# Optimization experiments

Measured on AMD Instinct MI355X. Metric: run time of the kernel, lower is better.

## Reference

```python
import jax, jax.numpy as jnp
import numpy as np

TOP_K = 2
SCALING = 32.0 / 16.0  # lora_alpha / r

N, D, O = 4096, 4096, 4096   # tokens, in_features, out_features
E, H, R_RANK = 8, 3, 16      # experts, B-heads per expert, lora rank
W_SCALE = 0.02               # keep logits in a sane range


def setup_inputs() -> dict:
    key = jax.random.key(0)
    ks = jax.random.split(key, 6)
    return {
        "x": jax.random.normal(ks[0], (N, D), jnp.float32),
        "base_W": jax.random.normal(ks[1], (D, O), jnp.float32) * W_SCALE,
        "router_W": jax.random.normal(ks[2], (E, D), jnp.float32) * W_SCALE,
        "A": jax.random.normal(ks[3], (E, D, R_RANK), jnp.float32) * W_SCALE,
        "B": jax.random.normal(ks[4], (E, H, R_RANK, O), jnp.float32) * W_SCALE,
        "R": jax.random.normal(ks[5], (E, D, H), jnp.float32) * W_SCALE,
    }


def reference(x, base_W, router_W, A, B, R):
    # Base dense layer
    base = x @ base_W                                   # [N, O]
    # Expert router: softmax over experts, top-k gate renormalized
    probs = jax.nn.softmax(x @ router_W.T, axis=-1)     # [N, E]
    topv, topi = jax.lax.top_k(probs, TOP_K)            # [N, k]
    topv = topv / topv.sum(-1, keepdims=True)
    n_idx = jnp.arange(x.shape[0])[:, None]
    gate = jnp.zeros_like(probs).at[n_idx, topi].set(topv)  # dense [N, E] gate, 0 off top-k
    # Shared lora_A per expert
    a = jnp.einsum('nd,edr->ner', x, A)                 # [N, E, r]
    # Per-expert head router over lora_B heads
    head_w = jax.nn.softmax(jnp.einsum('nd,edh->neh', x, R), axis=-1)  # [N, E, H]
    # Head-weighted B projections, combined with expert gates
    delta = jnp.einsum('ner,neh,ehro,ne->no', a, head_w, B, gate)      # [N, O]
    return base + SCALING * delta
```

## Files before the change

kernel.cpp:

```cpp
#include <hip/hip_runtime.h>
#include <hip/hip_bf16.h>
#include <math.h>

typedef __bf16 bf16_t;
typedef __bf16 bf16x4_t __attribute__((ext_vector_type(4)));
typedef __bf16 bf16x8_t __attribute__((ext_vector_type(8)));
typedef float  f32x4_t  __attribute__((ext_vector_type(4)));

#define N_TOK 4096
#define D_IN  4096
#define O_OUT 4096
#define NEXP  8
#define NHEAD 3
#define RANK  16
#define KC2   384
#define PCOLS 256
#define NKZ   8
#define SCALING_F 2.0f


__device__ __forceinline__ void transpose_tile(const float* __restrict__ src,
                                               bf16_t* __restrict__ dst,
                                               int Rr, int Cc, int r0, int c0,
                                               float (*tile)[65]) {
  int q  = threadIdx.x & 15;
  int r4 = threadIdx.x >> 4;
  #pragma unroll
  for (int g = 0; g < 4; ++g) {
    int r = r4 + g * 16;
    float4 v = *(const float4*)(src + (size_t)(r0 + r) * Cc + c0 + q * 4);
    tile[r][q * 4 + 0] = v.x; tile[r][q * 4 + 1] = v.y;
    tile[r][q * 4 + 2] = v.z; tile[r][q * 4 + 3] = v.w;
  }
  __syncthreads();
  int j  = threadIdx.x & 7;
  int cc = threadIdx.x >> 3;
  #pragma unroll
  for (int h = 0; h < 2; ++h) {
    int c = cc + h * 32;
    bf16x8_t o;
    #pragma unroll
    for (int i = 0; i < 8; ++i) o[i] = (bf16_t)tile[j * 8 + i][c];
    *(bf16x8_t*)(dst + (size_t)(c0 + c) * Rr + r0 + j * 8) = o;
  }
}

__global__ __launch_bounds__(256) void prep_kernel(const float* __restrict__ x,
                                                   const float* __restrict__ base_W,
                                                   const float* __restrict__ rw,
                                                   const float* __restrict__ A,
                                                   const float* __restrict__ B,
                                                   const float* __restrict__ Rm,
                                                   bf16_t* __restrict__ xb,
                                                   bf16_t* __restrict__ WbT,
                                                   bf16_t* __restrict__ BbT,
                                                   bf16_t* __restrict__ PabT,
                                                   int* __restrict__ gidx,
                                                   float* __restrict__ gwv) {
  __shared__ float tile[64][65];
  int b = blockIdx.x;
  if (b < 4096) {
    transpose_tile(base_W, WbT, 4096, 4096, (b & 63) * 64, (b >> 6) * 64, tile);
  } else if (b < 5120) {
    int lane = threadIdx.x & 63;
    int wv = threadIdx.x >> 6;
    int n = (b - 4096) * 4 + wv;
    const float4* xv = (const float4*)(x + (size_t)n * D_IN);
    bf16x4_t* xo = (bf16x4_t*)(xb + (size_t)n * D_IN);
    float acc[NEXP] = {0, 0, 0, 0, 0, 0, 0, 0};
    for (int d = lane; d < D_IN / 4; d += 64) {
      float4 xx = xv[d];
      bf16x4_t ob = { (bf16_t)xx.x, (bf16_t)xx.y, (bf16_t)xx.z, (bf16_t)xx.w };
      xo[d] = ob;
      #pragma unroll
      for (int e = 0; e < NEXP; ++e) {
        float4 ww = ((const float4*)(rw + (size_t)e * D_IN))[d];
        acc[e] += xx.x * ww.x + xx.y * ww.y + xx.z * ww.z + xx.w * ww.w;
      }
    }
    #pragma unroll
    for (int e = 0; e < NEXP; ++e) {
      float v = acc[e];
      #pragma unroll
      for (int o = 32; o > 0; o >>= 1) v += __shfl_down(v, o);
      acc[e] = v;
    }
    if (lane == 0) {
      int i0 = 0; float l0 = acc[0];
      #pragma unroll
      for (int e = 1; e < NEXP; ++e) if (acc[e] > l0) { l0 = acc[e]; i0 = e; }
      int i1 = -1; float l1 = -3.4e38f;
      #pragma unroll
      for (int e = 0; e < NEXP; ++e) if (e != i0 && acc[e] > l1) { l1 = acc[e]; i1 = e; }
      float w0 = 1.f / (1.f + expf(l1 - l0));
      gidx[2 * n] = i0; gidx[2 * n + 1] = i1;
      gwv[2 * n] = w0;  gwv[2 * n + 1] = 1.f - w0;
    }
  } else if (b < 5504) {
    int t = b - 5120;
    transpose_tile(B, BbT, KC2, 4096, (t % 6) * 64, (t / 6) * 64, tile);
  } else {
    int c = b - 5504;
    for (int d = threadIdx.x; d < D_IN; d += 256) {
      float v = 0.f;
      if (c < 128) {
        int e = c >> 4, r = c & 15;
        v = A[((size_t)e * D_IN + d) * RANK + r];
      } else if (c < 152) {
        int qq = c - 128; int e = qq / 3, h = qq - 3 * e;
        v = Rm[((size_t)e * D_IN + d) * NHEAD + h];
      }
      PabT[(size_t)c * D_IN + d] = (bf16_t)v;
    }
  }
}

__global__ void gating_kernel(const float* __restrict__ projP, const int* __restrict__ gidx,
                              const float* __restrict__ gwv, bf16_t* __restrict__ C2b) {
  int n = blockIdx.x;
  int c = threadIdx.x;
  int e = c / 48;
  int h = (c % 48) / 16;
  int r = c & 15;
  int i0 = gidx[2 * n], i1 = gidx[2 * n + 1];
  float g = (e == i0) ? gwv[2 * n] : (e == i1) ? gwv[2 * n + 1] : 0.f;
  float val = 0.f;
  if (g != 0.f) {
    const float* p0 = projP + (size_t)n * PCOLS;
    const size_t S = (size_t)N_TOK * PCOLS;
    float h0 = 0.f, h1 = 0.f, h2 = 0.f, av = 0.f;
    #pragma unroll
    for (int z = 0; z < NKZ; ++z) {
      const float* pz = p0 + (size_t)z * S;
      h0 += pz[128 + e * 3 + 0];
      h1 += pz[128 + e * 3 + 1];
      h2 += pz[128 + e * 3 + 2];
      av += pz[e * 16 + r];
    }
    float mx = fmaxf(h0, fmaxf(h1, h2));
    float e0 = expf(h0 - mx), e1 = expf(h1 - mx), e2 = expf(h2 - mx);
    float hw = (h == 0 ? e0 : h == 1 ? e1 : e2) / (e0 + e1 + e2);
    val = SCALING_F * g * hw * av;
  }
  C2b[(size_t)n * KC2 + c] = (bf16_t)val;
}

__device__ __forceinline__ void run_kloop(f32x4_t (&acc)[4][4], bf16_t* sA, bf16_t* sB,
                                          const bf16_t* __restrict__ Ab, int lda,
                                          const bf16_t* __restrict__ Bb, int ldb, int K) {
  const int tid = threadIdx.x;
  const int lane = tid & 63;
  const int w = tid >> 6;
  const int wm = (w >> 1) * 64;
  const int wn = (w & 1) * 64;
  const int qd = lane >> 4;
  const int ln = lane & 15;
  const int sw = ln & 7;

  size_t offA[4], offB[4];
  int lo[4];
  #pragma unroll
  for (int t = 0; t < 4; ++t) {
    int c = tid + t * 256;
    int m = c >> 3, kc = (c & 7) ^ (m & 7);
    offA[t] = (size_t)m * lda + kc * 8;
    offB[t] = (size_t)m * ldb + kc * 8;
    lo[t] = c * 8;
  }
  int rowA[4], rowB[4];
  #pragma unroll
  for (int i = 0; i < 4; ++i) {
    rowA[i] = (wm + i * 16 + ln) * 64;
    rowB[i] = (wn + i * 16 + ln) * 64;
  }

  for (int k0 = 0; k0 < K; k0 += 64) {
    __syncthreads();
    #pragma unroll
    for (int t = 0; t < 4; ++t)
      __builtin_amdgcn_global_load_lds(
          (const __attribute__((address_space(1))) void*)(Ab + k0 + offA[t]),
          (__attribute__((address_space(3))) void*)(sA + lo[t]), 16, 0, 0);
    #pragma unroll
    for (int t = 0; t < 4; ++t)
      __builtin_amdgcn_global_load_lds(
          (const __attribute__((address_space(1))) void*)(Bb + k0 + offB[t]),
          (__attribute__((address_space(3))) void*)(sB + lo[t]), 16, 0, 0);
    __syncthreads();
    #pragma unroll
    for (int s = 0; s < 2; ++s) {
      bf16x8_t af[4], bfr[4];
      int kx = ((s * 4 + qd) ^ sw) * 8;
      #pragma unroll
      for (int i = 0; i < 4; ++i) af[i]  = *(const bf16x8_t*)(sA + rowA[i] + kx);
      #pragma unroll
      for (int i = 0; i < 4; ++i) bfr[i] = *(const bf16x8_t*)(sB + rowB[i] + kx);
      #pragma unroll
      for (int i = 0; i < 4; ++i)
        #pragma unroll
        for (int j = 0; j < 4; ++j)
          acc[i][j] = __builtin_amdgcn_mfma_f32_16x16x32_bf16(af[i], bfr[j], acc[i][j], 0, 0, 0);
    }
  }
}

__global__ __launch_bounds__(256) void gemm_proj_kernel(const bf16_t* __restrict__ xb,
                                                        const bf16_t* __restrict__ PabT,
                                                        float* __restrict__ projP) {
  __shared__ bf16_t sA[128 * 64];
  __shared__ bf16_t sB[128 * 64];
  int bm = blockIdx.x, bn = blockIdx.y, kz = blockIdx.z;
  f32x4_t acc[4][4] = {};
  run_kloop(acc, sA, sB,
            xb + (size_t)bm * 128 * D_IN + kz * 512, D_IN,
            PabT + (size_t)bn * 128 * D_IN + kz * 512, D_IN, 512);
  const int lane = threadIdx.x & 63, w = threadIdx.x >> 6;
  const int wm = (w >> 1) * 64, wn = (w & 1) * 64, qd = lane >> 4, ln = lane & 15;
  float* Cb = projP + (size_t)kz * N_TOK * PCOLS + (size_t)bm * 128 * PCOLS + bn * 128;
  #pragma unroll
  for (int i = 0; i < 4; ++i)
    #pragma unroll
    for (int j = 0; j < 4; ++j) {
      int col = wn + j * 16 + ln;
      #pragma unroll
      for (int rg = 0; rg < 4; ++rg) {
        int row = wm + i * 16 + qd * 4 + rg;
        Cb[(size_t)row * PCOLS + col] = acc[i][j][rg];
      }
    }
}


#define SLOT 32768

__device__ __forceinline__ void stage4(const bf16_t* __restrict__ G, int k0,
                                       bf16_t* lbase, const size_t (&g)[4], int tid) {
  #pragma unroll
  for (int i = 0; i < 4; ++i)
    __builtin_amdgcn_global_load_lds(
        (const __attribute__((address_space(1))) void*)(G + g[i] + k0),
        (__attribute__((address_space(3))) void*)(lbase + (i * 512 + tid) * 8), 16, 0, 0);
}

template <int MB>
__device__ __forceinline__ void mfma16(f32x4_t (&acc)[8][4], const bf16x8_t (&af)[4],
                                       const bf16x8_t (&bv)[4]) {
  __builtin_amdgcn_s_setprio(1);
  #pragma unroll
  for (int mi = 0; mi < 4; ++mi)
    #pragma unroll
    for (int nj = 0; nj < 4; ++nj)
      acc[MB + mi][nj] =
          __builtin_amdgcn_mfma_f32_16x16x32_bf16(af[mi], bv[nj], acc[MB + mi][nj], 0, 0, 0);
  __builtin_amdgcn_s_setprio(0);
}

__device__ __forceinline__ void substep64(f32x4_t (&acc)[8][4], const bf16_t* pA,
                                          const bf16_t* pB, int kx) {
  bf16x8_t bv[4], a0[4], a1[4];
  #pragma unroll
  for (int nj = 0; nj < 4; ++nj) bv[nj] = *(const bf16x8_t*)(pB + nj * 1024 + kx);
  #pragma unroll
  for (int mi = 0; mi < 4; ++mi) a0[mi] = *(const bf16x8_t*)(pA + mi * 1024 + kx);
  mfma16<0>(acc, a0, bv);
  #pragma unroll
  for (int mi = 0; mi < 4; ++mi) a1[mi] = *(const bf16x8_t*)(pA + (4 + mi) * 1024 + kx);
  mfma16<4>(acc, a1, bv);
}

template <int SC>
__device__ __forceinline__ void tbody64(f32x4_t (&acc)[8][4], bf16_t* sring,
                                        const bf16_t* __restrict__ A,
                                        const bf16_t* __restrict__ B, int k1,
                                        const size_t (&gA)[4], const size_t (&gB)[4],
                                        int aoff, int boff, int kx0, int kx1, int tid) {
  stage4(A, k1, sring + (SC ^ 1) * SLOT, gA, tid);
  asm volatile("s_waitcnt vmcnt(4)" ::: "memory");
  __builtin_amdgcn_s_barrier();
  const bf16_t* pA = sring + SC * SLOT + aoff;
  const bf16_t* pB = sring + SC * SLOT + 16384 + boff;
  bf16x8_t bv[4], a0[4], a1[4];
  #pragma unroll
  for (int nj = 0; nj < 4; ++nj) bv[nj] = *(const bf16x8_t*)(pB + nj * 1024 + kx0);
  #pragma unroll
  for (int mi = 0; mi < 4; ++mi) a0[mi] = *(const bf16x8_t*)(pA + mi * 1024 + kx0);
  stage4(B, k1, sring + (SC ^ 1) * SLOT + 16384, gB, tid);
  mfma16<0>(acc, a0, bv);
  #pragma unroll
  for (int mi = 0; mi < 4; ++mi) a1[mi] = *(const bf16x8_t*)(pA + (4 + mi) * 1024 + kx0);
  mfma16<4>(acc, a1, bv);
  __builtin_amdgcn_s_barrier();
  substep64(acc, pA, pB, kx1);
  __builtin_amdgcn_sched_barrier(0);
  __builtin_amdgcn_s_barrier();
}

__device__ __forceinline__ void tail64(f32x4_t (&acc)[8][4], const bf16_t* slotbase,
                                       int aoff, int boff, int kx0, int kx1) {
  asm volatile("s_waitcnt vmcnt(0)" ::: "memory");
  __builtin_amdgcn_s_barrier();
  const bf16_t* pA = slotbase + aoff;
  const bf16_t* pB = slotbase + 16384 + boff;
  substep64(acc, pA, pB, kx0);
  __builtin_amdgcn_s_barrier();
  substep64(acc, pA, pB, kx1);
  __builtin_amdgcn_sched_barrier(0);
  __builtin_amdgcn_s_barrier();
}

__device__ __forceinline__ void kloop64(f32x4_t (&acc)[8][4], bf16_t* sring,
                                        const bf16_t* __restrict__ A, int lda,
                                        const bf16_t* __restrict__ B, int ldb,
                                        int K, int tid, int aoff, int boff,
                                        int kx0, int kx1) {
  size_t gA[4], gB[4];
  #pragma unroll
  for (int i = 0; i < 4; ++i) {
    int s = i * 512 + tid;
    int row = s >> 3;
    int c = (s & 7) ^ (row & 7);
    gA[i] = (size_t)row * lda + c * 8;
    gB[i] = (size_t)row * ldb + c * 8;
  }
  const int T = K / 64;
  stage4(A, 0, sring, gA, tid);
  stage4(B, 0, sring + 16384, gB, tid);
  int t = 0;
  for (; t + 1 < T - 1; t += 2) {
    tbody64<0>(acc, sring, A, B, (t + 1) * 64, gA, gB, aoff, boff, kx0, kx1, tid);
    tbody64<1>(acc, sring, A, B, (t + 2) * 64, gA, gB, aoff, boff, kx0, kx1, tid);
  }
  for (; t < T - 1; ++t) {
    if (t & 1) tbody64<1>(acc, sring, A, B, (t + 1) * 64, gA, gB, aoff, boff, kx0, kx1, tid);
    else       tbody64<0>(acc, sring, A, B, (t + 1) * 64, gA, gB, aoff, boff, kx0, kx1, tid);
  }
  tail64(acc, sring + ((T - 1) & 1) * SLOT, aoff, boff, kx0, kx1);
}

__global__ __launch_bounds__(512, 1) void gemm_fused256(const bf16_t* __restrict__ xb,
                                                        const bf16_t* __restrict__ WbT,
                                                        const bf16_t* __restrict__ C2b,
                                                        const bf16_t* __restrict__ BbT,
                                                        float* __restrict__ out) {
  __shared__ __align__(16) bf16_t sring[2 * SLOT];
  const int tid = threadIdx.x;
  const int lane = tid & 63;
  const int w = tid >> 6;
  const int wm = w >> 2;
  const int wn = w & 3;
  const int qd = lane >> 4;
  const int ln = lane & 15;

  int b = blockIdx.x;
  int sw = (b & 7) * 32 + (b >> 3);
  int bm = sw >> 4, bn = sw & 15;

  const int aoff = (wm * 128 + ln) * 64;
  const int boff = (wn * 64 + ln) * 64;
  const int kx0 = ((qd) ^ (ln & 7)) * 8;
  const int kx1 = ((4 + qd) ^ (ln & 7)) * 8;

  f32x4_t acc[8][4] = {};

  kloop64(acc, sring, xb  + (size_t)bm * 256 * D_IN, D_IN,
                      WbT + (size_t)bn * 256 * D_IN, D_IN, D_IN, tid, aoff, boff, kx0, kx1);
  kloop64(acc, sring, C2b + (size_t)bm * 256 * KC2,  KC2,
                      BbT + (size_t)bn * 256 * KC2,  KC2,  KC2,  tid, aoff, boff, kx0, kx1);

  float* Cb = out + (size_t)(bm * 256 + wm * 128) * O_OUT + bn * 256 + wn * 64;
  #pragma unroll
  for (int mi = 0; mi < 8; ++mi)
    #pragma unroll
    for (int nj = 0; nj < 4; ++nj)
      #pragma unroll
      for (int rg = 0; rg < 4; ++rg)
        Cb[(size_t)(mi * 16 + qd * 4 + rg) * O_OUT + nj * 16 + ln] = acc[mi][nj][rg];
}

extern "C" void kernel_launch(void* const* d_in, const int* in_sizes, int n_in,
                              void* d_out, int out_size, void* d_ws, size_t ws_size,
                              hipStream_t stream) {
  const float* x       = (const float*)d_in[0];
  const float* base_W  = (const float*)d_in[1];
  const float* routerW = (const float*)d_in[2];
  const float* A       = (const float*)d_in[3];
  const float* B       = (const float*)d_in[4];
  const float* Rm      = (const float*)d_in[5];
  float* out = (float*)d_out;
  char* ws = (char*)d_ws;

  bf16_t* xb   = (bf16_t*)(ws);
  bf16_t* WbT  = (bf16_t*)(ws + 33554432);
  bf16_t* PabT = (bf16_t*)(ws + 67108864);
  bf16_t* BbT  = (bf16_t*)(ws + 69206016);
  bf16_t* C2b  = (bf16_t*)(ws + 72351744);
  int*    gidx = (int*)   (ws + 75497472);
  float*  gwv  = (float*) (ws + 75530240);
  float*  projP = out;

  prep_kernel<<<5760, 256, 0, stream>>>(x, base_W, routerW, A, B, Rm,
                                        xb, WbT, BbT, PabT, gidx, gwv);
  gemm_proj_kernel<<<dim3(32, 2, NKZ), 256, 0, stream>>>(xb, PabT, projP);
  gating_kernel<<<4096, 384, 0, stream>>>(projP, gidx, gwv, C2b);
  gemm_fused256<<<dim3(256), 512, 0, stream>>>(xb, WbT, C2b, BbT, out);
}
```

Measured before the change: 356.2 us.

## Restructure fused GEMM main loop into 4-stage K=32 LDS pipeline with register prefetch

Replaces the double-buffered 64-wide K tile loop with a four-slot ring of 32-wide K tiles that keeps three stages in flight, and prefetches the next tile's A/B fragments into registers at the end of each step. The LDS swizzle is changed to match the narrower 32-element rows. The aim is to hide global-to-LDS latency better and overlap LDS reads with MFMA work. The cost is twice as many barriers per unit of K and more VGPR pressure from the prefetched fragments. The loop is now specialised at compile time on K, which must give a tile count divisible by four.

```diff
diff --git a/kernel.cpp b/kernel.cpp
--- a/kernel.cpp
+++ b/kernel.cpp
@@ -231,15 +231,21 @@
 }
 
 
-#define SLOT 32768
-
-__device__ __forceinline__ void stage4(const bf16_t* __restrict__ G, int k0,
-                                       bf16_t* lbase, const size_t (&g)[4], int tid) {
-  #pragma unroll
-  for (int i = 0; i < 4; ++i)
-    __builtin_amdgcn_global_load_lds(
-        (const __attribute__((address_space(1))) void*)(G + g[i] + k0),
-        (__attribute__((address_space(3))) void*)(lbase + (i * 512 + tid) * 8), 16, 0, 0);
+__device__ __forceinline__ void stage2(const bf16_t* __restrict__ G, int k0,
+                                       bf16_t* lbase, size_t g0, size_t g1, int tid) {
+  __builtin_amdgcn_global_load_lds(
+      (const __attribute__((address_space(1))) void*)(G + g0 + k0),
+      (__attribute__((address_space(3))) void*)(lbase + tid * 8), 16, 0, 0);
+  __builtin_amdgcn_global_load_lds(
+      (const __attribute__((address_space(1))) void*)(G + g1 + k0),
+      (__attribute__((address_space(3))) void*)(lbase + 4096 + tid * 8), 16, 0, 0);
+}
+
+template <int N>
+__device__ __forceinline__ void vm_wait() {
+  if constexpr (N == 8)      asm volatile("s_waitcnt vmcnt(8)" ::: "memory");
+  else if constexpr (N == 4) asm volatile("s_waitcnt vmcnt(4)" ::: "memory");
+  else if constexpr (N == 0) asm volatile("s_waitcnt vmcnt(0)" ::: "memory");
 }
 
 template <int MB>
@@ -255,86 +261,77 @@
   __builtin_amdgcn_s_setprio(0);
 }
 
-__device__ __forceinline__ void substep64(f32x4_t (&acc)[8][4], const bf16_t* pA,
-                                          const bf16_t* pB, int kx) {
-  bf16x8_t bv[4], a0[4], a1[4];
-  #pragma unroll
-  for (int nj = 0; nj < 4; ++nj) bv[nj] = *(const bf16x8_t*)(pB + nj * 1024 + kx);
-  #pragma unroll
-  for (int mi = 0; mi < 4; ++mi) a0[mi] = *(const bf16x8_t*)(pA + mi * 1024 + kx);
+template <int SC, bool STAGE, int VMN, bool NEXTRD>
+__device__ __forceinline__ void tbodyP(f32x4_t (&acc)[8][4], bf16_t* sring,
+                                       const bf16_t* __restrict__ Ag,
+                                       const bf16_t* __restrict__ Bg, int k3,
+                                       size_t gA0, size_t gA1, size_t gB0, size_t gB1,
+                                       int aoff, int boff, int tid,
+                                       bf16x8_t (&bv)[4], bf16x8_t (&a0)[4]) {
+  constexpr int SS = (SC + 3) & 3;
+  constexpr int SN = (SC + 1) & 3;
+  if constexpr (STAGE) stage2(Ag, k3, sring + SS * 16384, gA0, gA1, tid);
+  const bf16_t* pA = sring + SC * 16384 + aoff;
+  bf16x8_t a1[4];
   mfma16<0>(acc, a0, bv);
   #pragma unroll
-  for (int mi = 0; mi < 4; ++mi) a1[mi] = *(const bf16x8_t*)(pA + (4 + mi) * 1024 + kx);
+  for (int mi = 0; mi < 4; ++mi) a1[mi] = *(const bf16x8_t*)(pA + (4 + mi) * 512);
+  if constexpr (STAGE) stage2(Bg, k3, sring + SS * 16384 + 8192, gB0, gB1, tid);
+  vm_wait<VMN>();
+  __builtin_amdgcn_s_barrier();
   mfma16<4>(acc, a1, bv);
-}
-
-template <int SC>
-__device__ __forceinline__ void tbody64(f32x4_t (&acc)[8][4], bf16_t* sring,
-                                        const bf16_t* __restrict__ A,
-                                        const bf16_t* __restrict__ B, int k1,
-                                        const size_t (&gA)[4], const size_t (&gB)[4],
-                                        int aoff, int boff, int kx0, int kx1, int tid) {
-  stage4(A, k1, sring + (SC ^ 1) * SLOT, gA, tid);
-  asm volatile("s_waitcnt vmcnt(4)" ::: "memory");
-  __builtin_amdgcn_s_barrier();
-  const bf16_t* pA = sring + SC * SLOT + aoff;
-  const bf16_t* pB = sring + SC * SLOT + 16384 + boff;
-  bf16x8_t bv[4], a0[4], a1[4];
-  #pragma unroll
-  for (int nj = 0; nj < 4; ++nj) bv[nj] = *(const bf16x8_t*)(pB + nj * 1024 + kx0);
-  #pragma unroll
-  for (int mi = 0; mi < 4; ++mi) a0[mi] = *(const bf16x8_t*)(pA + mi * 1024 + kx0);
-  stage4(B, k1, sring + (SC ^ 1) * SLOT + 16384, gB, tid);
-  mfma16<0>(acc, a0, bv);
-  #pragma unroll
-  for (int mi = 0; mi < 4; ++mi) a1[mi] = *(const bf16x8_t*)(pA + (4 + mi) * 1024 + kx0);
-  mfma16<4>(acc, a1, bv);
-  __builtin_amdgcn_s_barrier();
-  substep64(acc, pA, pB, kx1);
+  if constexpr (NEXTRD) {
+    const bf16_t* qA = sring + SN * 16384 + aoff;
+    const bf16_t* qB = sring + SN * 16384 + 8192 + boff;
+    #pragma unroll
+    for (int nj = 0; nj < 4; ++nj) bv[nj] = *(const bf16x8_t*)(qB + nj * 512);
+    #pragma unroll
+    for (int mi = 0; mi < 4; ++mi) a0[mi] = *(const bf16x8_t*)(qA + mi * 512);
+  }
   __builtin_amdgcn_sched_barrier(0);
   __builtin_amdgcn_s_barrier();
 }
 
-__device__ __forceinline__ void tail64(f32x4_t (&acc)[8][4], const bf16_t* slotbase,
-                                       int aoff, int boff, int kx0, int kx1) {
-  asm volatile("s_waitcnt vmcnt(0)" ::: "memory");
+template <int K>
+__device__ __forceinline__ void kloopP(f32x4_t (&acc)[8][4], bf16_t* sring,
+                                       const bf16_t* __restrict__ A, int lda,
+                                       const bf16_t* __restrict__ B, int ldb,
+                                       int tid, int aoff, int boff) {
+  constexpr int T = K / 32;
+  static_assert((T & 3) == 0, "T must be multiple of 4");
+  const int s0 = tid,       r0 = s0 >> 2, c0 = (s0 & 3) ^ ((r0 >> 1) & 3);
+  const int s1 = 512 + tid, r1 = s1 >> 2, c1 = (s1 & 3) ^ ((r1 >> 1) & 3);
+  const size_t gA0 = (size_t)r0 * lda + c0 * 8, gA1 = (size_t)r1 * lda + c1 * 8;
+  const size_t gB0 = (size_t)r0 * ldb + c0 * 8, gB1 = (size_t)r1 * ldb + c1 * 8;
+
+  #pragma unroll
+  for (int t = 0; t < 3; ++t) {
+    stage2(A, t * 32, sring + t * 16384, gA0, gA1, tid);
+    stage2(B, t * 32, sring + t * 16384 + 8192, gB0, gB1, tid);
+  }
+  asm volatile("s_waitcnt vmcnt(8)" ::: "memory");
   __builtin_amdgcn_s_barrier();
-  const bf16_t* pA = slotbase + aoff;
-  const bf16_t* pB = slotbase + 16384 + boff;
-  substep64(acc, pA, pB, kx0);
-  __builtin_amdgcn_s_barrier();
-  substep64(acc, pA, pB, kx1);
-  __builtin_amdgcn_sched_barrier(0);
-  __builtin_amdgcn_s_barrier();
-}
-
-__device__ __forceinline__ void kloop64(f32x4_t (&acc)[8][4], bf16_t* sring,
-                                        const bf16_t* __restrict__ A, int lda,
-                                        const bf16_t* __restrict__ B, int ldb,
-                                        int K, int tid, int aoff, int boff,
-                                        int kx0, int kx1) {
-  size_t gA[4], gB[4];
-  #pragma unroll
-  for (int i = 0; i < 4; ++i) {
-    int s = i * 512 + tid;
-    int row = s >> 3;
-    int c = (s & 7) ^ (row & 7);
-    gA[i] = (size_t)row * lda + c * 8;
-    gB[i] = (size_t)row * ldb + c * 8;
-  }
-  const int T = K / 64;
-  stage4(A, 0, sring, gA, tid);
-  stage4(B, 0, sring + 16384, gB, tid);
+  bf16x8_t bv[4], a0[4];
+  {
+    const bf16_t* qA = sring + aoff;
+    const bf16_t* qB = sring + 8192 + boff;
+    #pragma unroll
+    for (int nj = 0; nj < 4; ++nj) bv[nj] = *(const bf16x8_t*)(qB + nj * 512);
+    #pragma unroll
+    for (int mi = 0; mi < 4; ++mi) a0[mi] = *(const bf16x8_t*)(qA + mi * 512);
+  }
+  constexpr int TM = T - 3;
   int t = 0;
-  for (; t + 1 < T - 1; t += 2) {
-    tbody64<0>(acc, sring, A, B, (t + 1) * 64, gA, gB, aoff, boff, kx0, kx1, tid);
-    tbody64<1>(acc, sring, A, B, (t + 2) * 64, gA, gB, aoff, boff, kx0, kx1, tid);
-  }
-  for (; t < T - 1; ++t) {
-    if (t & 1) tbody64<1>(acc, sring, A, B, (t + 1) * 64, gA, gB, aoff, boff, kx0, kx1, tid);
-    else       tbody64<0>(acc, sring, A, B, (t + 1) * 64, gA, gB, aoff, boff, kx0, kx1, tid);
-  }
-  tail64(acc, sring + ((T - 1) & 1) * SLOT, aoff, boff, kx0, kx1);
+  for (; t + 3 < TM; t += 4) {
+    tbodyP<0,true,8,true>(acc, sring, A, B, (t+3)*32, gA0,gA1,gB0,gB1, aoff,boff,tid, bv,a0);
+    tbodyP<1,true,8,true>(acc, sring, A, B, (t+4)*32, gA0,gA1,gB0,gB1, aoff,boff,tid, bv,a0);
+    tbodyP<2,true,8,true>(acc, sring, A, B, (t+5)*32, gA0,gA1,gB0,gB1, aoff,boff,tid, bv,a0);
+    tbodyP<3,true,8,true>(acc, sring, A, B, (t+6)*32, gA0,gA1,gB0,gB1, aoff,boff,tid, bv,a0);
+  }
+  tbodyP<0,true,8,true>(acc, sring, A, B, (t+3)*32, gA0,gA1,gB0,gB1, aoff,boff,tid, bv,a0);
+  tbodyP<1,false,4,true >(acc, sring, A, B, 0, gA0,gA1,gB0,gB1, aoff,boff,tid, bv,a0);
+  tbodyP<2,false,0,true >(acc, sring, A, B, 0, gA0,gA1,gB0,gB1, aoff,boff,tid, bv,a0);
+  tbodyP<3,false,-1,false>(acc, sring, A, B, 0, gA0,gA1,gB0,gB1, aoff,boff,tid, bv,a0);
 }
 
 __global__ __launch_bounds__(512, 1) void gemm_fused256(const bf16_t* __restrict__ xb,
@@ -342,7 +339,7 @@
                                                         const bf16_t* __restrict__ C2b,
                                                         const bf16_t* __restrict__ BbT,
                                                         float* __restrict__ out) {
-  __shared__ __align__(16) bf16_t sring[2 * SLOT];
+  __shared__ __align__(16) bf16_t sring[4 * 16384];
   const int tid = threadIdx.x;
   const int lane = tid & 63;
   const int w = tid >> 6;
@@ -350,22 +347,21 @@
   const int wn = w & 3;
   const int qd = lane >> 4;
   const int ln = lane & 15;
+  const int swz8 = ((qd ^ ((ln >> 1) & 3)) << 3);
 
   int b = blockIdx.x;
   int sw = (b & 7) * 32 + (b >> 3);
   int bm = sw >> 4, bn = sw & 15;
 
-  const int aoff = (wm * 128 + ln) * 64;
-  const int boff = (wn * 64 + ln) * 64;
-  const int kx0 = ((qd) ^ (ln & 7)) * 8;
-  const int kx1 = ((4 + qd) ^ (ln & 7)) * 8;
+  const int aoff = (wm * 128 + ln) * 32 + swz8;
+  const int boff = (wn * 64 + ln) * 32 + swz8;
 
   f32x4_t acc[8][4] = {};
 
-  kloop64(acc, sring, xb  + (size_t)bm * 256 * D_IN, D_IN,
-                      WbT + (size_t)bn * 256 * D_IN, D_IN, D_IN, tid, aoff, boff, kx0, kx1);
-  kloop64(acc, sring, C2b + (size_t)bm * 256 * KC2,  KC2,
-                      BbT + (size_t)bn * 256 * KC2,  KC2,  KC2,  tid, aoff, boff, kx0, kx1);
+  kloopP<D_IN>(acc, sring, xb  + (size_t)bm * 256 * D_IN, D_IN,
+                           WbT + (size_t)bn * 256 * D_IN, D_IN, tid, aoff, boff);
+  kloopP<KC2>(acc, sring, C2b + (size_t)bm * 256 * KC2,  KC2,
+                          BbT + (size_t)bn * 256 * KC2,  KC2,  tid, aoff, boff);
 
   float* Cb = out + (size_t)(bm * 256 + wm * 128) * O_OUT + bn * 256 + wn * 64;
   #pragma unroll
```

Result: faster. 348.0 us, median of 4 (-2.3%).
